# Performance work log

Hardware: AMD Instinct MI355X
Metric: run time of the kernel (lower is better)

## Reference

```python
import jax, jax.numpy as jnp
import numpy as np

K = 256      # model / per-head dim (module uses full k per head)
H = 8        # heads
B = 4
T = 2048
EPS = 1e-5   # nn.LayerNorm default eps


def _layernorm(x, gamma, beta):
    mu = jnp.mean(x, axis=-1, keepdims=True)
    var = jnp.mean(jnp.square(x - mu), axis=-1, keepdims=True)
    return (x - mu) * jax.lax.rsqrt(var + EPS) * gamma + beta


def setup_inputs() -> dict:
    key = jax.random.key(0)
    ks = jax.random.split(key, 12)
    s = lambda fan_in: 1.0 / np.sqrt(fan_in)
    return {
        "x":  jax.random.normal(ks[0], (B, T, K), dtype=jnp.float32),
        # attention projections, stored (in, out) for x @ W
        "wq": jax.random.uniform(ks[1], (K, K * H), jnp.float32, -s(K), s(K)),
        "wk": jax.random.uniform(ks[2], (K, K * H), jnp.float32, -s(K), s(K)),
        "wv": jax.random.uniform(ks[3], (K, K * H), jnp.float32, -s(K), s(K)),
        "wu": jax.random.uniform(ks[4], (K * H, K), jnp.float32, -s(K * H), s(K * H)),
        "bu": jnp.zeros((K,), jnp.float32),
        # feed-forward
        "w1": jax.random.uniform(ks[5], (K, 4 * K), jnp.float32, -s(K), s(K)),
        "b1": jnp.zeros((4 * K,), jnp.float32),
        "w2": jax.random.uniform(ks[6], (4 * K, K), jnp.float32, -s(4 * K), s(4 * K)),
        "b2": jnp.zeros((K,), jnp.float32),
        # layernorms
        "g1": jnp.ones((K,), jnp.float32),
        "be1": jnp.zeros((K,), jnp.float32),
        "g2": jnp.ones((K,), jnp.float32),
        "be2": jnp.zeros((K,), jnp.float32),
    }


def reference(x, wq, wk, wv, wu, bu, w1, b1, w2, b2, g1, be1, g2, be2):
    b, t, k = x.shape
    h = H
    scale = k ** (-0.25)  # applied to both q and k, as in the torch code
    q = (x @ wq).reshape(b, t, h, k).transpose(0, 2, 1, 3) * scale  # bhtk
    kk = (x @ wk).reshape(b, t, h, k).transpose(0, 2, 1, 3) * scale
    v = (x @ wv).reshape(b, t, h, k).transpose(0, 2, 1, 3)
    dot = jnp.einsum("bhtk,bhsk->bhts", q, kk)
    # masked=True: upper triangle (offset=1) set to -inf -> causal
    causal = jnp.tril(jnp.ones((t, t), dtype=bool))
    dot = jnp.where(causal, dot, -jnp.inf)
    attn = jax.nn.softmax(dot, axis=-1)
    out = jnp.einsum("bhts,bhsk->bhtk", attn, v)
    out = out.transpose(0, 2, 1, 3).reshape(b, t, h * k)
    attn_out = out @ wu + bu

    x = x + attn_out                    # residual=True
    x = _layernorm(x, g1, be1)          # norm=True
    ff = jnp.maximum(x @ w1 + b1, 0.0) @ w2 + b2
    x = x + ff                          # ff + residual
    x = _layernorm(x, g2, be2)
    return x
```

## Files before the change

kernel.cpp:

```cpp
#include <hip/hip_runtime.h>
#include <hip/hip_bf16.h>

#define TT 2048
#define BB 4
#define HH 8
#define KK 256
#define MM (BB*TT)
#define NQKV 6144
#define QKS 4096

typedef __attribute__((ext_vector_type(8))) short bf16x8;
typedef __attribute__((ext_vector_type(4))) float f32x4;

__device__ __forceinline__ void gld_lds16(const void* g, void* lds) {
    __builtin_amdgcn_global_load_lds(
        (const __attribute__((address_space(1))) unsigned int*)g,
        (__attribute__((address_space(3))) unsigned int*)lds, 16, 0, 0);
}

__global__ __launch_bounds__(256) void cvt_k(const float* __restrict__ in,
                                             __hip_bfloat16* __restrict__ out, int n) {
    int i = (blockIdx.x * 256 + threadIdx.x) * 4;
    if (i + 3 < n) {
        float4 v = *(const float4*)(in + i);
        out[i + 0] = __float2bfloat16(v.x);
        out[i + 1] = __float2bfloat16(v.y);
        out[i + 2] = __float2bfloat16(v.z);
        out[i + 3] = __float2bfloat16(v.w);
    }
}

__global__ __launch_bounds__(256) void transpose_cvt(const float* __restrict__ in,
                                                     __hip_bfloat16* __restrict__ out,
                                                     int R, int C) {
    __shared__ float tile[32][33];
    int c0 = blockIdx.x * 32, r0 = blockIdx.y * 32;
    int tx = threadIdx.x & 31, ty = threadIdx.x >> 5;
    #pragma unroll
    for (int i = ty; i < 32; i += 8)
        tile[i][tx] = in[(size_t)(r0 + i) * C + c0 + tx];
    __syncthreads();
    #pragma unroll
    for (int i = ty; i < 32; i += 8)
        out[(size_t)(c0 + i) * R + r0 + tx] = __float2bfloat16(tile[tx][i]);
}

template<int EPI, int BN>
__global__ __launch_bounds__(256) void gemm_k(const __hip_bfloat16* __restrict__ A,
                                              const __hip_bfloat16* __restrict__ Bt,
                                              int M, int N, int Kd,
                                              const float* __restrict__ bias,
                                              const float* __restrict__ res,
                                              void* __restrict__ outp, float scale,
                                              __hip_bfloat16* __restrict__ vtp) {
    __shared__ short sA[128 * 32];
    __shared__ short sB[BN * 32];
    int tid = threadIdx.x, lane = tid & 63, wave = tid >> 6;
    int l15 = lane & 15, g = lane >> 4;
    int m0 = blockIdx.y * 128, n0 = blockIdx.x * BN;
    constexpr int NF = BN / 32;
    int wm = (wave >> 1) * 64, wn = (wave & 1) * (BN / 2);
    f32x4 acc[4][NF] = {};
    const int NT = Kd >> 5;

    int arow0 = tid >> 2, acol = (tid & 3) * 8;
    int arow1 = (tid + 256) >> 2;

    for (int kt = 0; kt < NT; ++kt) {
        size_t ka = (size_t)kt * 32 + acol;
        gld_lds16(A + (size_t)(m0 + arow0) * Kd + ka, (char*)sA + wave * 1024);
        gld_lds16(A + (size_t)(m0 + arow1) * Kd + ka, (char*)sA + 4096 + wave * 1024);
        gld_lds16(Bt + (size_t)(n0 + arow0) * Kd + ka, (char*)sB + wave * 1024);
        if (BN == 128)
            gld_lds16(Bt + (size_t)(n0 + arow1) * Kd + ka, (char*)sB + 4096 + wave * 1024);
        asm volatile("s_waitcnt vmcnt(0)" ::: "memory");
        __syncthreads();
        bf16x8 af[4], bfr[NF];
        #pragma unroll
        for (int mf = 0; mf < 4; ++mf)
            af[mf] = *(const bf16x8*)&sA[(wm + mf * 16 + l15) * 32 + g * 8];
        #pragma unroll
        for (int nf = 0; nf < NF; ++nf)
            bfr[nf] = *(const bf16x8*)&sB[(wn + nf * 16 + l15) * 32 + g * 8];
        #pragma unroll
        for (int mf = 0; mf < 4; ++mf)
            #pragma unroll
            for (int nf = 0; nf < NF; ++nf)
                acc[mf][nf] = __builtin_amdgcn_mfma_f32_16x16x32_bf16(af[mf], bfr[nf], acc[mf][nf], 0, 0, 0);
        __syncthreads();
    }

    #pragma unroll
    for (int mf = 0; mf < 4; ++mf) {
        int rowb = m0 + wm + mf * 16 + g * 4;
        #pragma unroll
        for (int nf = 0; nf < NF; ++nf) {
            int col = n0 + wn + nf * 16 + l15;
            if (EPI == 0) {
                if (col < 4096) {
                    #pragma unroll
                    for (int r = 0; r < 4; ++r)
                        ((__hip_bfloat16*)outp)[(size_t)(rowb + r) * QKS + col] =
                            __float2bfloat16(acc[mf][nf][r] * scale);
                } else {
                    int hv = col - 4096, h = hv >> 8, d = hv & 255;
                    int b = rowb >> 11, t = rowb & 2047;
                    ushort4 w;
                    w.x = __bfloat16_as_ushort(__float2bfloat16(acc[mf][nf][0]));
                    w.y = __bfloat16_as_ushort(__float2bfloat16(acc[mf][nf][1]));
                    w.z = __bfloat16_as_ushort(__float2bfloat16(acc[mf][nf][2]));
                    w.w = __bfloat16_as_ushort(__float2bfloat16(acc[mf][nf][3]));
                    *(ushort4*)(vtp + ((size_t)((b * 8 + h) * 256 + d)) * TT + t) = w;
                }
            } else {
                #pragma unroll
                for (int r = 0; r < 4; ++r) {
                    float v = acc[mf][nf][r];
                    size_t idx = (size_t)(rowb + r) * N + col;
                    if (EPI == 1) {
                        ((float*)outp)[idx] = v + bias[col] + res[idx];
                    } else {
                        v += bias[col];
                        ((__hip_bfloat16*)outp)[idx] = __float2bfloat16(v > 0.0f ? v : 0.0f);
                    }
                }
            }
        }
    }
}

__global__ __launch_bounds__(512, 2) void attn_k(const __hip_bfloat16* __restrict__ QK,
                                                 const __hip_bfloat16* __restrict__ VT,
                                                 __hip_bfloat16* __restrict__ O) {
    __shared__ char Kl[2][32768];
    __shared__ char Vl[2][32768];
    __shared__ char Pl[8][2048];
    int tid = threadIdx.x, lane = tid & 63, wave = tid >> 6;
    int id = blockIdx.x;
    int xcd = id & 7, w = id >> 3;
    int bh = xcd * 4 + (w >> 3);
    int jtp = w & 7;
    int b = bh >> 3, h = bh & 7;
    const __hip_bfloat16* Qb = QK + (size_t)b * TT * QKS + h * KK;
    const __hip_bfloat16* Kb = Qb + 2048;
    const __hip_bfloat16* Vtb = VT + (size_t)bh * KK * TT;

    int l15 = lane & 15, g = lane >> 4;
    int koff = g * 8;
    int koffB = g * 16;
    int pswz = (l15 & 7) << 4;

    auto STAGE = [&](int s0, int buf) {
        #pragma unroll
        for (int rd = 0; rd < 4; ++rd) {
            int L = rd * 8192 + tid * 16;
            int row = L >> 9;
            int cb = (L & 511) ^ ((row & 7) << 4);
            gld_lds16((const char*)(Kb + (size_t)(s0 + row) * QKS) + cb,
                      Kl[buf] + rd * 8192 + wave * 1024);
        }
        #pragma unroll
        for (int rd = 0; rd < 4; ++rd) {
            int L = rd * 8192 + tid * 16;
            int row = L >> 7;
            int cb = (L & 127) ^ ((row & 7) << 4);
            gld_lds16((const char*)(Vtb + (size_t)row * TT + s0) + cb,
                      Vl[buf] + rd * 8192 + wave * 1024);
        }
    };

    #pragma unroll 1
    for (int half = 0; half < 2; ++half) {
        int jt = (half == 0) ? jtp : 15 - jtp;
        int q0 = jt * 128;
        int rowbase = q0 + wave * 16;
        bf16x8 qf[8];
        #pragma unroll
        for (int kk = 0; kk < 8; ++kk)
            qf[kk] = *(const bf16x8*)(Qb + (size_t)(rowbase + l15) * QKS + kk * 32 + koff);

        f32x4 Oa[16] = {};
        float mrow = -__builtin_inff();
        float lrow = 0.f;

        STAGE(0, 0);
        asm volatile("s_waitcnt vmcnt(0)" ::: "memory");
        __syncthreads();
        int cur = 0;
        const int niter = 2 * jt + 2;

        #pragma unroll 1
        for (int i = 0; i < niter; ++i) {
            int s0 = i * 64;
            if (i + 1 < niter) STAGE(s0 + 64, cur ^ 1);

            if (s0 <= rowbase + 15) {
                f32x4 S[4] = {};
                __builtin_amdgcn_s_setprio(1);
                #pragma unroll
                for (int nf = 0; nf < 4; ++nf) {
                    int r = nf * 16 + l15;
                    int swz = (r & 7) << 4;
                    #pragma unroll
                    for (int kk = 0; kk < 8; ++kk) {
                        bf16x8 kf = *(const bf16x8*)(Kl[cur] + r * 512 + ((kk * 64 + koffB) ^ swz));
                        S[nf] = __builtin_amdgcn_mfma_f32_16x16x32_bf16(kf, qf[kk], S[nf], 0, 0, 0);
                    }
                }
                __builtin_amdgcn_s_setprio(0);
                if (s0 + 63 > rowbase) {
                    int qg = rowbase + l15;
                    #pragma unroll
                    for (int nf = 0; nf < 4; ++nf)
                        #pragma unroll
                        for (int r = 0; r < 4; ++r) {
                            int sg = s0 + nf * 16 + g * 4 + r;
                            if (sg > qg) S[nf][r] = -__builtin_inff();
                        }
                }
                float mx = S[0][0];
                #pragma unroll
                for (int nf = 0; nf < 4; ++nf)
                    #pragma unroll
                    for (int r = 0; r < 4; ++r) mx = fmaxf(mx, S[nf][r]);
                mx = fmaxf(mx, __shfl_xor(mx, 16));
                mx = fmaxf(mx, __shfl_xor(mx, 32));
                if (__any(mx > mrow + 8.0f)) {
                    float mn = fmaxf(mrow, mx);
                    float alpha = exp2f(mrow - mn);
                    mrow = mn;
                    lrow *= alpha;
                    float al[4];
                    #pragma unroll
                    for (int r = 0; r < 4; ++r) al[r] = __shfl(alpha, (g << 2) + r);
                    #pragma unroll
                    for (int nf2 = 0; nf2 < 16; ++nf2)
                        #pragma unroll
                        for (int r = 0; r < 4; ++r) Oa[nf2][r] *= al[r];
                }
                float ps = 0.f;
                #pragma unroll
                for (int nf = 0; nf < 4; ++nf)
                    #pragma unroll
                    for (int r = 0; r < 4; ++r) {
                        float p = exp2f(S[nf][r] - mrow);
                        S[nf][r] = p; ps += p;
                    }
                ps += __shfl_xor(ps, 16);
                ps += __shfl_xor(ps, 32);
                lrow += ps;
                #pragma unroll
                for (int nf = 0; nf < 4; ++nf) {
                    uint2 pk2;
                    pk2.x = (unsigned)__bfloat16_as_ushort(__float2bfloat16(S[nf][0]))
                          | ((unsigned)__bfloat16_as_ushort(__float2bfloat16(S[nf][1])) << 16);
                    pk2.y = (unsigned)__bfloat16_as_ushort(__float2bfloat16(S[nf][2]))
                          | ((unsigned)__bfloat16_as_ushort(__float2bfloat16(S[nf][3])) << 16);
                    *(uint2*)(Pl[wave] + l15 * 128 + ((nf * 32 + g * 8) ^ pswz)) = pk2;
                }
                bf16x8 pa[2];
                #pragma unroll
                for (int kk2 = 0; kk2 < 2; ++kk2)
                    pa[kk2] = *(const bf16x8*)(Pl[wave] + l15 * 128 + ((kk2 * 64 + koffB) ^ pswz));
                __builtin_amdgcn_s_setprio(1);
                #pragma unroll
                for (int nf2 = 0; nf2 < 16; ++nf2) {
                    int r = nf2 * 16 + l15;
                    int swz = (r & 7) << 4;
                    #pragma unroll
                    for (int kk2 = 0; kk2 < 2; ++kk2) {
                        bf16x8 vb = *(const bf16x8*)(Vl[cur] + r * 128 + ((kk2 * 64 + koffB) ^ swz));
                        Oa[nf2] = __builtin_amdgcn_mfma_f32_16x16x32_bf16(pa[kk2], vb, Oa[nf2], 0, 0, 0);
                    }
                }
                __builtin_amdgcn_s_setprio(0);
            }
            asm volatile("s_waitcnt vmcnt(0)" ::: "memory");
            __syncthreads();
            cur ^= 1;
        }
        float rcp_ = 1.0f / lrow;
        float rc[4];
        #pragma unroll
        for (int r = 0; r < 4; ++r) rc[r] = __shfl(rcp_, (g << 2) + r);
        #pragma unroll
        for (int nf2 = 0; nf2 < 16; ++nf2) {
            int col = nf2 * 16 + l15;
            #pragma unroll
            for (int r = 0; r < 4; ++r) {
                int t = rowbase + g * 4 + r;
                O[((size_t)b * TT + t) * 2048 + h * KK + col] = __float2bfloat16(Oa[nf2][r] * rc[r]);
            }
        }
    }
}

__global__ __launch_bounds__(256) void layernorm_k(const float* __restrict__ y,
                                                   const float* __restrict__ g,
                                                   const float* __restrict__ be,
                                                   float* __restrict__ out_f,
                                                   __hip_bfloat16* __restrict__ out_b) {
    int row = blockIdx.x * 4 + (threadIdx.x >> 6);
    int lane = threadIdx.x & 63;
    float4 v = *(const float4*)(y + (size_t)row * 256 + lane * 4);
    float s = v.x + v.y + v.z + v.w;
    #pragma unroll
    for (int d = 1; d < 64; d <<= 1) s += __shfl_xor(s, d);
    float mu = s * (1.0f / 256.0f);
    float dx = v.x - mu, dy = v.y - mu, dz = v.z - mu, dw = v.w - mu;
    float q = dx * dx + dy * dy + dz * dz + dw * dw;
    #pragma unroll
    for (int d = 1; d < 64; d <<= 1) q += __shfl_xor(q, d);
    float rs = rsqrtf(q * (1.0f / 256.0f) + 1e-5f);
    float4 gg = *(const float4*)(g + lane * 4);
    float4 bb = *(const float4*)(be + lane * 4);
    float4 o;
    o.x = dx * rs * gg.x + bb.x;
    o.y = dy * rs * gg.y + bb.y;
    o.z = dz * rs * gg.z + bb.z;
    o.w = dw * rs * gg.w + bb.w;
    *(float4*)(out_f + (size_t)row * 256 + lane * 4) = o;
    if (out_b) {
        size_t i = (size_t)row * 256 + lane * 4;
        out_b[i + 0] = __float2bfloat16(o.x);
        out_b[i + 1] = __float2bfloat16(o.y);
        out_b[i + 2] = __float2bfloat16(o.z);
        out_b[i + 3] = __float2bfloat16(o.w);
    }
}

extern "C" void kernel_launch(void* const* d_in, const int* in_sizes, int n_in,
                              void* d_out, int out_size, void* d_ws, size_t ws_size,
                              hipStream_t stream) {
    const float* x  = (const float*)d_in[0];
    const float* wq = (const float*)d_in[1];
    const float* wk = (const float*)d_in[2];
    const float* wv = (const float*)d_in[3];
    const float* wu = (const float*)d_in[4];
    const float* bu = (const float*)d_in[5];
    const float* w1 = (const float*)d_in[6];
    const float* b1 = (const float*)d_in[7];
    const float* w2 = (const float*)d_in[8];
    const float* b2 = (const float*)d_in[9];
    const float* g1 = (const float*)d_in[10];
    const float* be1 = (const float*)d_in[11];
    const float* g2 = (const float*)d_in[12];
    const float* be2 = (const float*)d_in[13];

    char* p = (char*)d_ws;
    auto alloc = [&](size_t bytes) { char* r = p; p += bytes; return r; };
    __hip_bfloat16* xb    = (__hip_bfloat16*)alloc((size_t)MM * KK * 2);
    __hip_bfloat16* wqkvT = (__hip_bfloat16*)alloc((size_t)NQKV * KK * 2);
    __hip_bfloat16* wuT   = (__hip_bfloat16*)alloc((size_t)KK * 2048 * 2);
    __hip_bfloat16* w1T   = (__hip_bfloat16*)alloc((size_t)1024 * KK * 2);
    __hip_bfloat16* w2T   = (__hip_bfloat16*)alloc((size_t)KK * 1024 * 2);
    __hip_bfloat16* qk    = (__hip_bfloat16*)alloc((size_t)MM * QKS * 2);
    __hip_bfloat16* vt    = (__hip_bfloat16*)alloc((size_t)32 * KK * TT * 2);
    __hip_bfloat16* attn  = (__hip_bfloat16*)alloc((size_t)MM * 2048 * 2);
    float*          y1    = (float*)alloc((size_t)MM * KK * 4);
    float*          x1    = (float*)alloc((size_t)MM * KK * 4);
    __hip_bfloat16* x1b   = (__hip_bfloat16*)alloc((size_t)MM * KK * 2);
    __hip_bfloat16* hid   = (__hip_bfloat16*)alloc((size_t)MM * 1024 * 2);
    float*          y2    = (float*)alloc((size_t)MM * KK * 4);

    cvt_k<<<(MM * KK) / 1024, 256, 0, stream>>>(x, xb, MM * KK);
    transpose_cvt<<<dim3(64, 8),  256, 0, stream>>>(wq, wqkvT,             256, 2048);
    transpose_cvt<<<dim3(64, 8),  256, 0, stream>>>(wk, wqkvT + 2048 * 256, 256, 2048);
    transpose_cvt<<<dim3(64, 8),  256, 0, stream>>>(wv, wqkvT + 4096 * 256, 256, 2048);
    transpose_cvt<<<dim3(8, 64),  256, 0, stream>>>(wu, wuT, 2048, 256);
    transpose_cvt<<<dim3(32, 8),  256, 0, stream>>>(w1, w1T, 256, 1024);
    transpose_cvt<<<dim3(8, 32),  256, 0, stream>>>(w2, w2T, 1024, 256);

    gemm_k<0, 128><<<dim3(NQKV / 128, MM / 128), 256, 0, stream>>>(
        xb, wqkvT, MM, NQKV, 256, nullptr, nullptr, qk, 0.3002806f, vt);

    attn_k<<<dim3(256), 512, 0, stream>>>(qk, vt, attn);

    gemm_k<1, 64><<<dim3(4, MM / 128), 256, 0, stream>>>(
        attn, wuT, MM, 256, 2048, bu, x, y1, 1.0f, nullptr);
    layernorm_k<<<MM / 4, 256, 0, stream>>>(y1, g1, be1, x1, x1b);

    gemm_k<2, 128><<<dim3(8, MM / 128), 256, 0, stream>>>(
        x1b, w1T, MM, 1024, 256, b1, nullptr, hid, 1.0f, nullptr);
    gemm_k<1, 64><<<dim3(4, MM / 128), 256, 0, stream>>>(
        hid, w2T, MM, 256, 1024, b2, x1, y2, 1.0f, nullptr);
    layernorm_k<<<MM / 4, 256, 0, stream>>>(y2, g2, be2, (float*)d_out, nullptr);
}
```

Before: 265.0 us.

## Rework attention kernel around 32x32x16 MFMA with both causal tiles per block

The attention kernel moves from 16x16x32 to 32x32x16 bf16 MFMA. Each wave now owns 32 query rows, and the first four waves take query tile jt while the last four take tile 15-jt. Both tiles run in one shared K/V streaming loop instead of two sequential halves, so the K/V blocks for the shorter tile are loaded once and reused by the longer tile. This aims to raise MFMA throughput per LDS read and cut redundant global-to-LDS staging, at the cost of more accumulator registers, new swizzle layouts and wave imbalance between the two tiles.

```diff
diff --git a/kernel.cpp b/kernel.cpp
--- a/kernel.cpp
+++ b/kernel.cpp
@@ -11,11 +11,17 @@
 
 typedef __attribute__((ext_vector_type(8))) short bf16x8;
 typedef __attribute__((ext_vector_type(4))) float f32x4;
+typedef __attribute__((ext_vector_type(16))) float f32x16;
 
 __device__ __forceinline__ void gld_lds16(const void* g, void* lds) {
     __builtin_amdgcn_global_load_lds(
         (const __attribute__((address_space(1))) unsigned int*)g,
         (__attribute__((address_space(3))) unsigned int*)lds, 16, 0, 0);
+}
+
+__device__ __forceinline__ unsigned pkbf(float a, float b) {
+    return (unsigned)__bfloat16_as_ushort(__float2bfloat16(a))
+         | ((unsigned)__bfloat16_as_ushort(__float2bfloat16(b)) << 16);
 }
 
 __global__ __launch_bounds__(256) void cvt_k(const float* __restrict__ in,
@@ -134,164 +140,144 @@
                                                  __hip_bfloat16* __restrict__ O) {
     __shared__ char Kl[2][32768];
     __shared__ char Vl[2][32768];
-    __shared__ char Pl[8][2048];
+    __shared__ char Pl[8][2560];
     int tid = threadIdx.x, lane = tid & 63, wave = tid >> 6;
+    int l31 = lane & 31, hi = lane >> 5;
     int id = blockIdx.x;
     int xcd = id & 7, w = id >> 3;
     int bh = xcd * 4 + (w >> 3);
-    int jtp = w & 7;
+    int jt = w & 7;
     int b = bh >> 3, h = bh & 7;
     const __hip_bfloat16* Qb = QK + (size_t)b * TT * QKS + h * KK;
     const __hip_bfloat16* Kb = Qb + 2048;
     const __hip_bfloat16* Vtb = VT + (size_t)bh * KK * TT;
 
-    int l15 = lane & 15, g = lane >> 4;
-    int koff = g * 8;
-    int koffB = g * 16;
-    int pswz = (l15 & 7) << 4;
+    int tile = (wave < 4) ? jt : 15 - jt;
+    int q0w = tile * 128 + (wave & 3) * 32;
+    int qg = q0w + l31;
+
+    bf16x8 qf[16];
+    #pragma unroll
+    for (int ks = 0; ks < 16; ++ks)
+        qf[ks] = *(const bf16x8*)(Qb + (size_t)qg * QKS + ks * 16 + hi * 8);
 
     auto STAGE = [&](int s0, int buf) {
         #pragma unroll
         for (int rd = 0; rd < 4; ++rd) {
-            int L = rd * 8192 + tid * 16;
-            int row = L >> 9;
-            int cb = (L & 511) ^ ((row & 7) << 4);
-            gld_lds16((const char*)(Kb + (size_t)(s0 + row) * QKS) + cb,
+            int s = rd * 16 + wave * 2 + hi;
+            int kg = l31 ^ ((s & 15) << 1);
+            gld_lds16((const char*)(Kb + (size_t)(s0 + s) * QKS) + kg * 16,
                       Kl[buf] + rd * 8192 + wave * 1024);
         }
         #pragma unroll
         for (int rd = 0; rd < 4; ++rd) {
-            int L = rd * 8192 + tid * 16;
-            int row = L >> 7;
-            int cb = (L & 127) ^ ((row & 7) << 4);
-            gld_lds16((const char*)(Vtb + (size_t)row * TT + s0) + cb,
+            int R = rd * 16 + wave * 2 + hi;
+            int v = l31 ^ ((R & 15) << 1);
+            int d = (v >> 3) * 64 + R;
+            gld_lds16((const char*)(Vtb + (size_t)d * TT + s0 + (v & 7) * 8),
                       Vl[buf] + rd * 8192 + wave * 1024);
         }
     };
 
+    f32x16 Oa[8] = {};
+    float mrow = -__builtin_inff();
+    float lrow = 0.f;
+
+    STAGE(0, 0);
+    asm volatile("s_waitcnt vmcnt(0)" ::: "memory");
+    __syncthreads();
+    int cur = 0;
+    const int niter = 2 * (16 - jt);
+
     #pragma unroll 1
-    for (int half = 0; half < 2; ++half) {
-        int jt = (half == 0) ? jtp : 15 - jtp;
-        int q0 = jt * 128;
-        int rowbase = q0 + wave * 16;
-        bf16x8 qf[8];
-        #pragma unroll
-        for (int kk = 0; kk < 8; ++kk)
-            qf[kk] = *(const bf16x8*)(Qb + (size_t)(rowbase + l15) * QKS + kk * 32 + koff);
-
-        f32x4 Oa[16] = {};
-        float mrow = -__builtin_inff();
-        float lrow = 0.f;
-
-        STAGE(0, 0);
-        asm volatile("s_waitcnt vmcnt(0)" ::: "memory");
-        __syncthreads();
-        int cur = 0;
-        const int niter = 2 * jt + 2;
-
-        #pragma unroll 1
-        for (int i = 0; i < niter; ++i) {
-            int s0 = i * 64;
-            if (i + 1 < niter) STAGE(s0 + 64, cur ^ 1);
-
-            if (s0 <= rowbase + 15) {
-                f32x4 S[4] = {};
+    for (int i = 0; i < niter; ++i) {
+        int s0 = i * 64;
+        if (i + 1 < niter) STAGE(s0 + 64, cur ^ 1);
+
+        if (s0 <= q0w + 31) {
+            #pragma unroll
+            for (int st = 0; st < 2; ++st) {
+                f32x16 S = {};
                 __builtin_amdgcn_s_setprio(1);
                 #pragma unroll
-                for (int nf = 0; nf < 4; ++nf) {
-                    int r = nf * 16 + l15;
-                    int swz = (r & 7) << 4;
+                for (int ks = 0; ks < 16; ++ks) {
+                    int r = st * 32 + l31;
+                    bf16x8 kf = *(const bf16x8*)(Kl[cur] + r * 512 +
+                                  (((ks * 2 + hi) << 4) ^ ((r & 15) << 5)));
+                    S = __builtin_amdgcn_mfma_f32_32x32x16_bf16(kf, qf[ks], S, 0, 0, 0);
+                }
+                __builtin_amdgcn_s_setprio(0);
+                if (s0 + st * 32 + 31 > q0w) {
                     #pragma unroll
-                    for (int kk = 0; kk < 8; ++kk) {
-                        bf16x8 kf = *(const bf16x8*)(Kl[cur] + r * 512 + ((kk * 64 + koffB) ^ swz));
-                        S[nf] = __builtin_amdgcn_mfma_f32_16x16x32_bf16(kf, qf[kk], S[nf], 0, 0, 0);
+                    for (int r = 0; r < 16; ++r) {
+                        int sg = s0 + st * 32 + (r & 3) + ((r >> 2) << 3) + hi * 4;
+                        if (sg > qg) S[r] = -__builtin_inff();
                     }
                 }
-                __builtin_amdgcn_s_setprio(0);
-                if (s0 + 63 > rowbase) {
-                    int qg = rowbase + l15;
-                    #pragma unroll
-                    for (int nf = 0; nf < 4; ++nf)
-                        #pragma unroll
-                        for (int r = 0; r < 4; ++r) {
-                            int sg = s0 + nf * 16 + g * 4 + r;
-                            if (sg > qg) S[nf][r] = -__builtin_inff();
-                        }
-                }
-                float mx = S[0][0];
-                #pragma unroll
-                for (int nf = 0; nf < 4; ++nf)
-                    #pragma unroll
-                    for (int r = 0; r < 4; ++r) mx = fmaxf(mx, S[nf][r]);
-                mx = fmaxf(mx, __shfl_xor(mx, 16));
+                float mx = S[0];
+                #pragma unroll
+                for (int r = 1; r < 16; ++r) mx = fmaxf(mx, S[r]);
                 mx = fmaxf(mx, __shfl_xor(mx, 32));
                 if (__any(mx > mrow + 8.0f)) {
                     float mn = fmaxf(mrow, mx);
                     float alpha = exp2f(mrow - mn);
                     mrow = mn;
                     lrow *= alpha;
-                    float al[4];
                     #pragma unroll
-                    for (int r = 0; r < 4; ++r) al[r] = __shfl(alpha, (g << 2) + r);
-                    #pragma unroll
-                    for (int nf2 = 0; nf2 < 16; ++nf2)
+                    for (int r = 0; r < 16; ++r) {
+                        float al = __shfl(alpha, (r & 3) + ((r >> 2) << 3) + hi * 4);
                         #pragma unroll
-                        for (int r = 0; r < 4; ++r) Oa[nf2][r] *= al[r];
+                        for (int dt = 0; dt < 8; ++dt) Oa[dt][r] *= al;
+                    }
                 }
                 float ps = 0.f;
                 #pragma unroll
-                for (int nf = 0; nf < 4; ++nf)
-                    #pragma unroll
-                    for (int r = 0; r < 4; ++r) {
-                        float p = exp2f(S[nf][r] - mrow);
-                        S[nf][r] = p; ps += p;
-                    }
-                ps += __shfl_xor(ps, 16);
+                for (int r = 0; r < 16; ++r) {
+                    float p = exp2f(S[r] - mrow);
+                    S[r] = p; ps += p;
+                }
                 ps += __shfl_xor(ps, 32);
                 lrow += ps;
                 #pragma unroll
-                for (int nf = 0; nf < 4; ++nf) {
+                for (int g2 = 0; g2 < 4; ++g2) {
                     uint2 pk2;
-                    pk2.x = (unsigned)__bfloat16_as_ushort(__float2bfloat16(S[nf][0]))
-                          | ((unsigned)__bfloat16_as_ushort(__float2bfloat16(S[nf][1])) << 16);
-                    pk2.y = (unsigned)__bfloat16_as_ushort(__float2bfloat16(S[nf][2]))
-                          | ((unsigned)__bfloat16_as_ushort(__float2bfloat16(S[nf][3])) << 16);
-                    *(uint2*)(Pl[wave] + l15 * 128 + ((nf * 32 + g * 8) ^ pswz)) = pk2;
+                    pk2.x = pkbf(S[g2 * 4 + 0], S[g2 * 4 + 1]);
+                    pk2.y = pkbf(S[g2 * 4 + 2], S[g2 * 4 + 3]);
+                    *(uint2*)(Pl[wave] + l31 * 80 + g2 * 16 + hi * 8) = pk2;
                 }
                 bf16x8 pa[2];
                 #pragma unroll
-                for (int kk2 = 0; kk2 < 2; ++kk2)
-                    pa[kk2] = *(const bf16x8*)(Pl[wave] + l15 * 128 + ((kk2 * 64 + koffB) ^ pswz));
+                for (int ks2 = 0; ks2 < 2; ++ks2)
+                    pa[ks2] = *(const bf16x8*)(Pl[wave] + l31 * 80 + ks2 * 32 + hi * 16);
                 __builtin_amdgcn_s_setprio(1);
                 #pragma unroll
-                for (int nf2 = 0; nf2 < 16; ++nf2) {
-                    int r = nf2 * 16 + l15;
-                    int swz = (r & 7) << 4;
+                for (int dt = 0; dt < 8; ++dt) {
+                    int R = (dt & 1) * 32 + l31;
                     #pragma unroll
-                    for (int kk2 = 0; kk2 < 2; ++kk2) {
-                        bf16x8 vb = *(const bf16x8*)(Vl[cur] + r * 128 + ((kk2 * 64 + koffB) ^ swz));
-                        Oa[nf2] = __builtin_amdgcn_mfma_f32_16x16x32_bf16(pa[kk2], vb, Oa[nf2], 0, 0, 0);
+                    for (int ks2 = 0; ks2 < 2; ++ks2) {
+                        int lg = ((dt >> 1) << 3) + st * 4 + ks2 * 2 + hi;
+                        bf16x8 vb = *(const bf16x8*)(Vl[cur] + R * 512 +
+                                      ((lg << 4) ^ ((R & 15) << 5)));
+                        Oa[dt] = __builtin_amdgcn_mfma_f32_32x32x16_bf16(pa[ks2], vb, Oa[dt], 0, 0, 0);
                     }
                 }
                 __builtin_amdgcn_s_setprio(0);
             }
-            asm volatile("s_waitcnt vmcnt(0)" ::: "memory");
-            __syncthreads();
-            cur ^= 1;
         }
-        float rcp_ = 1.0f / lrow;
-        float rc[4];
-        #pragma unroll
-        for (int r = 0; r < 4; ++r) rc[r] = __shfl(rcp_, (g << 2) + r);
-        #pragma unroll
-        for (int nf2 = 0; nf2 < 16; ++nf2) {
-            int col = nf2 * 16 + l15;
-            #pragma unroll
-            for (int r = 0; r < 4; ++r) {
-                int t = rowbase + g * 4 + r;
-                O[((size_t)b * TT + t) * 2048 + h * KK + col] = __float2bfloat16(Oa[nf2][r] * rc[r]);
-            }
-        }
+        asm volatile("s_waitcnt vmcnt(0)" ::: "memory");
+        __syncthreads();
+        cur ^= 1;
+    }
+    float rcp_ = 1.0f / lrow;
+    #pragma unroll
+    for (int r = 0; r < 16; ++r) {
+        int crow = (r & 3) + ((r >> 2) << 3) + hi * 4;
+        float rc = __shfl(rcp_, crow);
+        int t = q0w + crow;
+        __hip_bfloat16* op = O + ((size_t)b * TT + t) * 2048 + h * KK + l31;
+        #pragma unroll
+        for (int dt = 0; dt < 8; ++dt)
+            op[dt * 32] = __float2bfloat16(Oa[dt][r] * rc);
     }
 }
 
```

New measurement: 354.4 us. 33.7% more time.
